# Kernel optimization log

Hardware: AMD Instinct MI355X
Metric: run time of the kernel (lower is better)

## Reference

```python
import jax, jax.numpy as jnp
import numpy as np

N, NFEAT, NHID, NCLASS, NIDX = 200000, 512, 128, 70, 10000


def normalize_l2(X):
    # row L2-normalize; norm is detached in the original (stop_gradient),
    # inf scale (zero rows) mapped to 0
    rownorm = jax.lax.stop_gradient(jnp.linalg.norm(X, axis=1, keepdims=True))
    scale = jnp.where(rownorm > 0, 1.0 / rownorm, 0.0)
    return X * scale


def setup_inputs() -> dict:
    key = jax.random.key(0)
    ks = jax.random.split(key, 9)
    x = jax.random.normal(ks[0], (N, NFEAT), dtype=jnp.float32)
    simple_features = jax.random.normal(ks[1], (N, NFEAT), dtype=jnp.float32)
    idx = jax.random.randint(ks[2], (NIDX,), 0, N)
    s = 0.05
    W0 = jax.random.normal(ks[3], (NHID, NFEAT), dtype=jnp.float32) * s
    W1 = jax.random.normal(ks[4], (NHID, NFEAT), dtype=jnp.float32) * s
    G1 = jax.random.normal(ks[5], (NHID, NHID), dtype=jnp.float32) * s
    G2 = jax.random.normal(ks[6], (NHID, NHID), dtype=jnp.float32) * s
    GT = jax.random.normal(ks[7], (NHID, 2 * NHID), dtype=jnp.float32) * s
    Wc = jax.random.normal(ks[8], (NCLASS, NHID), dtype=jnp.float32) * s
    return {"x": x, "simple_features": simple_features, "idx": idx,
            "W0": W0, "W1": W1, "G1": G1, "G2": G2, "GT": GT, "Wc": Wc}


def reference(x, simple_features, idx, W0, W1, G1, G2, GT, Wc):
    x = normalize_l2(x)                      # [N, nfeat]
    sf = normalize_l2(simple_features)       # [N, nfeat]
    # dropout/dropout_adj are identity (p=0)
    layer_inner = jax.nn.relu(x @ W0.T)      # [N, nhid]
    lay_simple = jax.nn.relu(sf @ W1.T)      # [N, nhid]
    gate1 = layer_inner @ G1.T               # [N, nhid]
    gate2 = lay_simple @ G2.T                # [N, nhid]
    gate = jax.nn.sigmoid(jnp.concatenate([gate1, gate2], axis=1) @ GT.T)
    fix_inner = (1.0 - gate) * layer_inner + gate * lay_simple
    fix_inner = normalize_l2(fix_inner)
    logits = jax.nn.relu(fix_inner @ Wc.T)   # [N, nclass]
    return jax.nn.log_softmax(logits, axis=-1)[idx]
```

## Files before the change

### kernel.cpp

```cpp
#include <hip/hip_runtime.h>
#include <math.h>

#define NFEAT  512
#define NHID   128
#define NCLASS 70
#define NIDX   10000
#define NTILE  625
#define HELEMS (2u * NIDX * NHID)
#define GELEMS (2u * NIDX * NHID)
#define WIMG_ELEMS (2u * 128 * 512)
#define SMALL_ELEMS 74496u
#define WS_NEED ((size_t)(HELEMS + GELEMS + WIMG_ELEMS + SMALL_ELEMS) * 2)

typedef float  f32x4  __attribute__((ext_vector_type(4)));
typedef __bf16 bf16x8 __attribute__((ext_vector_type(8)));

static __device__ __forceinline__ unsigned short f2bf(float f) {
    unsigned u = __builtin_bit_cast(unsigned, f);
    u += 0x7fffu + ((u >> 16) & 1u);
    return (unsigned short)(u >> 16);
}
static __device__ __forceinline__ float bf2f(unsigned short h) {
    unsigned u = ((unsigned)h) << 16;
    return __builtin_bit_cast(float, u);
}
static __device__ __forceinline__ bf16x8 pack8(float4 a, float4 b) {
    bf16x8 r;
    r[0] = (__bf16)a.x; r[1] = (__bf16)a.y; r[2] = (__bf16)a.z; r[3] = (__bf16)a.w;
    r[4] = (__bf16)b.x; r[5] = (__bf16)b.y; r[6] = (__bf16)b.z; r[7] = (__bf16)b.w;
    return r;
}
static __device__ __forceinline__ bf16x8 pack8s(float4 a, float4 b, float s) {
    bf16x8 r;
    r[0] = (__bf16)(a.x * s); r[1] = (__bf16)(a.y * s); r[2] = (__bf16)(a.z * s); r[3] = (__bf16)(a.w * s);
    r[4] = (__bf16)(b.x * s); r[5] = (__bf16)(b.y * s); r[6] = (__bf16)(b.z * s); r[7] = (__bf16)(b.w * s);
    return r;
}
static __device__ __forceinline__ f32x4 MFMA(bf16x8 a, bf16x8 b, f32x4 c) {
    return __builtin_amdgcn_mfma_f32_16x16x32_bf16(a, b, c, 0, 0, 0);
}
static __device__ __forceinline__ bf16x8 ldsAx(const unsigned short* base, int row, int colb, int rstride) {
    return *(const bf16x8*)((const char*)base + row * rstride + (colb ^ ((row & 7) << 4)));
}
static __device__ __forceinline__ void ldsW1(unsigned short* base, int row, int col, unsigned short v) {
    *(unsigned short*)((char*)base + row * 256 + ((col * 2) ^ ((row & 7) << 4))) = v;
}
static __device__ __forceinline__ float ldsR1(const unsigned short* base, int row, int col) {
    return bf2f(*(const unsigned short*)((const char*)base + row * 256 + ((col * 2) ^ ((row & 7) << 4))));
}

__global__ void prep_weights(const float* __restrict__ W0, const float* __restrict__ W1,
                             const float* __restrict__ G1, const float* __restrict__ G2,
                             const float* __restrict__ GT, const float* __restrict__ Wc,
                             unsigned short* __restrict__ wsWimg,
                             unsigned short* __restrict__ wsSmall) {
    int i = blockIdx.x * 256 + threadIdx.x;
    if (i < 16384) {
        int t = i >> 13;
        int r = i & 8191;
        int n = r >> 6, k8 = r & 63;
        const float* src = (t ? W1 : W0) + (size_t)n * NFEAT + k8 * 8;
        float4 a = ((const float4*)src)[0], b = ((const float4*)src)[1];
        char* dst = (char*)wsWimg + t * 131072 + n * 1024 + ((k8 * 16) ^ ((n & 7) << 4));
        *(bf16x8*)dst = pack8(a, b);
    } else {
        int i4 = i - 16384;
        if (i4 >= 18624) return;
        const float* src; int base4, dstb;
        if      (i4 < 4096)  { src = G1; base4 = 0;     dstb = 0; }
        else if (i4 < 8192)  { src = G2; base4 = 4096;  dstb = 16384; }
        else if (i4 < 16384) { src = GT; base4 = 8192;  dstb = 32768; }
        else                 { src = Wc; base4 = 16384; dstb = 65536; }
        float4 v = ((const float4*)src)[i4 - base4];
        ushort4 o;
        o.x = f2bf(v.x); o.y = f2bf(v.y); o.z = f2bf(v.z); o.w = f2bf(v.w);
        *(ushort4*)(wsSmall + dstb + (size_t)(i4 - base4) * 4) = o;
    }
}

__global__ __launch_bounds__(512) void stageBC(
    const float* __restrict__ x, const float* __restrict__ sf,
    const int* __restrict__ idx,
    const unsigned short* __restrict__ wsWimg,
    const unsigned short* __restrict__ wsSmall,
    unsigned short* __restrict__ wsH,
    unsigned short* __restrict__ wsG)
{
    __shared__ __align__(16) unsigned short Wl[65536];
    __shared__ __align__(16) unsigned short Xl[8192];
    __shared__ __align__(16) unsigned short Hl[2048];
    __shared__ __align__(16) unsigned short Gl[2048];

    const int tid  = threadIdx.x;
    const int w    = tid >> 6;
    const int lane = tid & 63;
    const int ln   = lane & 15, lg = lane >> 4;
    const int bid  = blockIdx.x;
    const int t    = bid / 125, tb = bid % 125;
    const int tile0 = tb * 5;
    const float* XS = t ? sf : x;
    const f32x4 zero4 = {0.f, 0.f, 0.f, 0.f};

    float4 ga0, ga1, gb0, gb1;
    {
        int r0 = idx[tile0 * 16 + w];
        int r1 = idx[tile0 * 16 + w + 8];
        const float4* p0 = (const float4*)(XS + (size_t)r0 * NFEAT + lane * 8);
        const float4* p1 = (const float4*)(XS + (size_t)r1 * NFEAT + lane * 8);
        ga0 = p0[0]; ga1 = p0[1];
        gb0 = p1[0]; gb1 = p1[1];
    }
    bf16x8 cf[4];
    {
        const unsigned short* Gsm = wsSmall + t * 16384;
        #pragma unroll
        for (int kc = 0; kc < 4; ++kc)
            cf[kc] = *(const bf16x8*)(Gsm + (size_t)(w * 16 + ln) * NHID + kc * 32 + lg * 8);
    }
    {
        const uint4* src = (const uint4*)((const char*)wsWimg + (size_t)t * 131072);
        uint4* dst = (uint4*)Wl;
        #pragma unroll
        for (int i = 0; i < 16; ++i) dst[tid + i * 512] = src[tid + i * 512];
    }
    auto putX = [&](int m, float4 a, float4 b) {
        float ss = a.x*a.x + a.y*a.y + a.z*a.z + a.w*a.w
                 + b.x*b.x + b.y*b.y + b.z*b.z + b.w*b.w;
        #pragma unroll
        for (int d = 1; d < 64; d <<= 1) ss += __shfl_xor(ss, d);
        float scl = (ss > 0.f) ? (1.f / sqrtf(ss)) : 0.f;
        *(bf16x8*)((char*)Xl + m * 1024 + ((lane * 16) ^ ((m & 7) << 4))) = pack8s(a, b, scl);
    };
    putX(w,     ga0, ga1);
    putX(w + 8, gb0, gb1);
    __syncthreads();

    for (int it = 0; it < 5; ++it) {
        float4 na0, na1, nb0, nb1;
        if (it < 4) {
            int tile = tile0 + it + 1;
            int r0 = idx[tile * 16 + w];
            int r1 = idx[tile * 16 + w + 8];
            const float4* p0 = (const float4*)(XS + (size_t)r0 * NFEAT + lane * 8);
            const float4* p1 = (const float4*)(XS + (size_t)r1 * NFEAT + lane * 8);
            na0 = p0[0]; na1 = p0[1];
            nb0 = p1[0]; nb1 = p1[1];
        }
        f32x4 accE = zero4, accO = zero4;
        #pragma unroll
        for (int kc = 0; kc < 16; ++kc) {
            bf16x8 a = ldsAx(Xl, ln,          kc * 64 + lg * 16, 1024);
            bf16x8 b = ldsAx(Wl, w * 16 + ln, kc * 64 + lg * 16, 1024);
            if (kc & 1) accO = MFMA(a, b, accO); else accE = MFMA(a, b, accE);
        }
        f32x4 acc = accE + accO;
        #pragma unroll
        for (int rg = 0; rg < 4; ++rg)
            ldsW1(Hl, lg * 4 + rg, w * 16 + ln, f2bf(fmaxf(acc[rg], 0.f)));
        __syncthreads();

        f32x4 aC = zero4;
        #pragma unroll
        for (int kc = 0; kc < 4; ++kc) {
            bf16x8 a = ldsAx(Hl, ln, kc * 64 + lg * 16, 256);
            aC = MFMA(a, cf[kc], aC);
        }
        if (tid < 256) {
            int tile = tile0 + it;
            ((uint4*)(wsH + ((size_t)t * NIDX + (size_t)tile * 16) * NHID))[tid]
                = ((const uint4*)Hl)[tid];
        }
        if (it < 4) {
            putX(w,     na0, na1);
            putX(w + 8, nb0, nb1);
        }
        #pragma unroll
        for (int rg = 0; rg < 4; ++rg)
            ldsW1(Gl, lg * 4 + rg, w * 16 + ln, f2bf(aC[rg]));
        __syncthreads();

        if (tid < 256) {
            int tile = tile0 + it;
            ((uint4*)(wsG + ((size_t)t * NIDX + (size_t)tile * 16) * NHID))[tid]
                = ((const uint4*)Gl)[tid];
        }
    }
}

__global__ __launch_bounds__(512) void tailDE5(
    const unsigned short* __restrict__ wsSmall,
    const unsigned short* __restrict__ wsH,
    const unsigned short* __restrict__ wsG,
    float* __restrict__ out)
{
    __shared__ __align__(16) char SM[102400];
    __shared__ float scl2s[5][16];

    unsigned short* Hb = (unsigned short*)SM;
    unsigned short* Gb = (unsigned short*)(SM + 40960);
    unsigned short* FX = (unsigned short*)(SM + 81920);
    float* LOGb = (float*)SM;

    const unsigned short* GTp = wsSmall + 32768;
    const unsigned short* Wcp = wsSmall + 65536;

    const int tid  = threadIdx.x;
    const int w    = tid >> 6;
    const int lane = tid & 63;
    const int ln   = lane & 15, lg = lane >> 4;
    const int tile0 = blockIdx.x * 5;
    const f32x4 zero4 = {0.f, 0.f, 0.f, 0.f};

    #pragma unroll
    for (int i = 0; i < 5; ++i) {
        int q = tid + i * 512;
        int seg = q >> 8, r = q & 255;
        int ti = seg >> 1, tt = seg & 1;
        size_t off = ((size_t)tt * NIDX + (size_t)(tile0 + ti) * 16) * NHID;
        ((uint4*)Hb)[q] = ((const uint4*)(wsH + off))[r];
        ((uint4*)Gb)[q] = ((const uint4*)(wsG + off))[r];
    }
    const int nD = w * 16 + ln;
    bf16x8 gt[8];
    #pragma unroll
    for (int kc = 0; kc < 8; ++kc)
        gt[kc] = *(const bf16x8*)(GTp + (size_t)nD * (2 * NHID) + kc * 32 + lg * 8);
    const int ccE = nD;
    const int ccl = (ccE < NCLASS) ? ccE : 0;
    bf16x8 wcf[4];
    #pragma unroll
    for (int kc = 0; kc < 4; ++kc)
        wcf[kc] = *(const bf16x8*)(Wcp + (size_t)ccl * NHID + kc * 32 + lg * 8);
    __syncthreads();

    #pragma unroll
    for (int ti = 0; ti < 5; ++ti) {
        f32x4 aE = zero4, aO = zero4;
        #pragma unroll
        for (int kc = 0; kc < 8; ++kc) {
            const unsigned short* As = Gb + ti * 4096 + (kc >> 2) * 2048;
            bf16x8 a = ldsAx(As, ln, (kc & 3) * 64 + lg * 16, 256);
            if (kc & 1) aO = MFMA(a, gt[kc], aO); else aE = MFMA(a, gt[kc], aE);
        }
        f32x4 accD = aE + aO;
        #pragma unroll
        for (int rg = 0; rg < 4; ++rg) {
            int m = lg * 4 + rg;
            float g  = 1.f / (1.f + __expf(-accD[rg]));
            float h0 = ldsR1(Hb + ti * 4096,        m, nD);
            float h1 = ldsR1(Hb + ti * 4096 + 2048, m, nD);
            ldsW1(FX + ti * 2048, m, nD, f2bf((1.f - g) * h0 + g * h1));
        }
    }
    __syncthreads();

    {
        int rr = tid >> 4, sl = tid & 15;
        #pragma unroll
        for (int j = 0; j < 3; ++j) {
            int rs = j * 32 + rr;
            if (rs < 80) {
                int ti = rs >> 4, r = rs & 15;
                bf16x8 v = ldsAx(FX + ti * 2048, r, sl * 16, 256);
                float ss = 0.f;
                #pragma unroll
                for (int jj = 0; jj < 8; ++jj) { float f = (float)v[jj]; ss += f * f; }
                ss += __shfl_xor(ss, 1); ss += __shfl_xor(ss, 2);
                ss += __shfl_xor(ss, 4); ss += __shfl_xor(ss, 8);
                if (sl == 0) scl2s[ti][r] = (ss > 0.f) ? (1.f / sqrtf(ss)) : 0.f;
            }
        }
    }
    __syncthreads();

    if (w < 5) {
        const bool live = (ccE < NCLASS);
        bf16x8 bfz;
        #pragma unroll
        for (int j = 0; j < 8; ++j) bfz[j] = (__bf16)0.f;
        #pragma unroll
        for (int ti = 0; ti < 5; ++ti) {
            f32x4 accE = zero4;
            #pragma unroll
            for (int kc = 0; kc < 4; ++kc) {
                bf16x8 a = ldsAx(FX + ti * 2048, ln, kc * 64 + lg * 16, 256);
                accE = MFMA(a, live ? wcf[kc] : bfz, accE);
            }
            if (live) {
                float* LO = LOGb + ti * 1280;
                #pragma unroll
                for (int rg = 0; rg < 4; ++rg) {
                    int m = lg * 4 + rg;
                    LO[m * 80 + ccE] = fmaxf(accE[rg] * scl2s[ti][m], 0.f);
                }
            }
        }
    }
    __syncthreads();

    {
        int rr = tid >> 4, l16 = tid & 15;
        #pragma unroll
        for (int j = 0; j < 3; ++j) {
            int rs = j * 32 + rr;
            if (rs < 80) {
                int ti = rs >> 4, r = rs & 15;
                const float* LO = LOGb + ti * 1280 + r * 80;
                float v[5];
                #pragma unroll
                for (int jj = 0; jj < 5; ++jj) {
                    int c = l16 + jj * 16;
                    v[jj] = (c < NCLASS) ? LO[c] : -1e30f;
                }
                float mx = v[0];
                #pragma unroll
                for (int jj = 1; jj < 5; ++jj) mx = fmaxf(mx, v[jj]);
                mx = fmaxf(mx, __shfl_xor(mx, 1)); mx = fmaxf(mx, __shfl_xor(mx, 2));
                mx = fmaxf(mx, __shfl_xor(mx, 4)); mx = fmaxf(mx, __shfl_xor(mx, 8));
                float se = 0.f;
                #pragma unroll
                for (int jj = 0; jj < 5; ++jj) {
                    int c = l16 + jj * 16;
                    if (c < NCLASS) se += __expf(v[jj] - mx);
                }
                se += __shfl_xor(se, 1); se += __shfl_xor(se, 2);
                se += __shfl_xor(se, 4); se += __shfl_xor(se, 8);
                float lz = mx + __logf(se);
                size_t orow = (size_t)(tile0 + ti) * 16 + r;
                #pragma unroll
                for (int jj = 0; jj < 5; ++jj) {
                    int c = l16 + jj * 16;
                    if (c < NCLASS) out[orow * NCLASS + c] = v[jj] - lz;
                }
            }
        }
    }
}

static __device__ __forceinline__ bf16x8 bfragF(const float* p, size_t off) {
    const float4* q = (const float4*)(p + off);
    return pack8(q[0], q[1]);
}
__global__ __launch_bounds__(512) void hyper_fb(
    const float* __restrict__ x, const float* __restrict__ sf,
    const int* __restrict__ idx,
    const float* __restrict__ W0, const float* __restrict__ W1,
    const float* __restrict__ G1, const float* __restrict__ G2,
    const float* __restrict__ GT, const float* __restrict__ Wc,
    float* __restrict__ out)
{
    __shared__ __align__(16) unsigned short Xbuf[2][16][NFEAT];
    __shared__ __align__(16) unsigned short Hbuf[2][16][NHID];
    __shared__ float scl2[16];
    unsigned short* G12 = &Xbuf[0][0][0];
    unsigned short* FIX = &Xbuf[0][0][0] + 4096;
    float*          LOG = (float*)(&Xbuf[0][0][0] + 6144);

    const int tid = threadIdx.x, bid = blockIdx.x;
    const int w = tid >> 6, lane = tid & 63;
    const int ln = lane & 15, lg = lane >> 4;
    const int tB = w >> 2, nq = w & 3;
    const f32x4 zero4 = {0.f, 0.f, 0.f, 0.f};

    {
        char* xb = (char*)&Xbuf[0][0][0];
        #pragma unroll
        for (int j = 0; j < 4; ++j) {
            int p = w * 4 + j, t = p >> 4, m = p & 15;
            int ri = idx[bid * 16 + m];
            const float4* q = (const float4*)((t ? sf : x) + (size_t)ri * NFEAT + lane * 8);
            float4 a = q[0], b = q[1];
            float ss = a.x*a.x + a.y*a.y + a.z*a.z + a.w*a.w
                     + b.x*b.x + b.y*b.y + b.z*b.z + b.w*b.w;
            #pragma unroll
            for (int d = 1; d < 64; d <<= 1) ss += __shfl_xor(ss, d);
            float scl = (ss > 0.f) ? (1.f / sqrtf(ss)) : 0.f;
            int soff = t * 16384 + m * 1024 + ((lane * 16) ^ ((m & 7) << 4));
            *(bf16x8*)(xb + soff) = pack8s(a, b, scl);
        }
    }
    __syncthreads();
    {
        const float* Wp = tB ? W1 : W0;
        f32x4 acc0 = zero4, acc1 = zero4;
        const unsigned short* Xb = (const unsigned short*)((const char*)&Xbuf[0][0][0] + tB * 16384);
        #pragma unroll
        for (int kc = 0; kc < 16; ++kc) {
            bf16x8 a = ldsAx(Xb, ln, kc * 64 + lg * 16, 1024);
            acc0 = MFMA(a, bfragF(Wp, (size_t)(nq * 32 + ln) * NFEAT + kc * 32 + lg * 8), acc0);
            acc1 = MFMA(a, bfragF(Wp, (size_t)(nq * 32 + 16 + ln) * NFEAT + kc * 32 + lg * 8), acc1);
        }
        unsigned short* Hb = &Hbuf[tB][0][0];
        #pragma unroll
        for (int rg = 0; rg < 4; ++rg) {
            int m = lg * 4 + rg;
            ldsW1(Hb, m, nq * 32 + ln,      f2bf(fmaxf(acc0[rg], 0.f)));
            ldsW1(Hb, m, nq * 32 + 16 + ln, f2bf(fmaxf(acc1[rg], 0.f)));
        }
    }
    __syncthreads();
    {
        const float* Gp = tB ? G2 : G1;
        const unsigned short* Hs = &Hbuf[tB][0][0];
        f32x4 accC[2] = {zero4, zero4};
        #pragma unroll
        for (int kc = 0; kc < 4; ++kc) {
            bf16x8 a = ldsAx(Hs, ln, kc * 64 + lg * 16, 256);
            accC[0] = MFMA(a, bfragF(Gp, (size_t)(nq * 32 + ln) * NHID + kc * 32 + lg * 8), accC[0]);
            accC[1] = MFMA(a, bfragF(Gp, (size_t)(nq * 32 + 16 + ln) * NHID + kc * 32 + lg * 8), accC[1]);
        }
        unsigned short* Gd = G12 + tB * 2048;
        #pragma unroll
        for (int nt = 0; nt < 2; ++nt)
            #pragma unroll
            for (int rg = 0; rg < 4; ++rg) {
                int m = lg * 4 + rg;
                ldsW1(Gd, m, nq * 32 + nt * 16 + ln, f2bf(accC[nt][rg]));
            }
    }
    __syncthreads();
    {
        f32x4 accD = zero4;
        const int n = w * 16 + ln;
        #pragma unroll
        for (int kc = 0; kc < 8; ++kc) {
            const unsigned short* As = G12 + (kc >> 2) * 2048;
            bf16x8 a = ldsAx(As, ln, (kc & 3) * 64 + lg * 16, 256);
            accD = MFMA(a, bfragF(GT, (size_t)n * (2 * NHID) + kc * 32 + lg * 8), accD);
        }
        #pragma unroll
        for (int rg = 0; rg < 4; ++rg) {
            int m = lg * 4 + rg;
            float g  = 1.f / (1.f + __expf(-accD[rg]));
            float h0 = ldsR1(&Hbuf[0][0][0], m, n);
            float h1 = ldsR1(&Hbuf[1][0][0], m, n);
            ldsW1(FIX, m, n, f2bf((1.f - g) * h0 + g * h1));
        }
    }
    __syncthreads();
    if (tid < 256) {
        int r = tid >> 4, sl = tid & 15;
        bf16x8 v = ldsAx(FIX, r, sl * 16, 256);
        float ss = 0.f;
        #pragma unroll
        for (int j = 0; j < 8; ++j) { float f = (float)v[j]; ss += f * f; }
        ss += __shfl_xor(ss, 1); ss += __shfl_xor(ss, 2);
        ss += __shfl_xor(ss, 4); ss += __shfl_xor(ss, 8);
        if (sl == 0) scl2[r] = (ss > 0.f) ? (1.f / sqrtf(ss)) : 0.f;
    }
    __syncthreads();
    if (w < 5) {
        const int cc = w * 16 + ln;
        bf16x8 bfz;
        #pragma unroll
        for (int j = 0; j < 8; ++j) bfz[j] = (__bf16)0.f;
        f32x4 accE = zero4;
        #pragma unroll
        for (int kc = 0; kc < 4; ++kc) {
            bf16x8 a = ldsAx(FIX, ln, kc * 64 + lg * 16, 256);
            bf16x8 b = (cc < NCLASS) ? bfragF(Wc, (size_t)cc * NHID + kc * 32 + lg * 8) : bfz;
            accE = MFMA(a, b, accE);
        }
        #pragma unroll
        for (int rg = 0; rg < 4; ++rg) {
            int m = lg * 4 + rg;
            float v = fmaxf(accE[rg] * scl2[m], 0.f);
            LOG[m * 80 + cc] = (cc < NCLASS) ? v : -1e30f;
        }
    }
    __syncthreads();
    {
        const int r = tid >> 5, l32 = tid & 31;
        float v0 = LOG[r * 80 + l32];
        float v1 = LOG[r * 80 + 32 + l32];
        float v2 = (l32 < 16) ? LOG[r * 80 + 64 + l32] : -1e30f;
        float mx = fmaxf(fmaxf(v0, v1), v2);
        #pragma unroll
        for (int d = 1; d < 32; d <<= 1) mx = fmaxf(mx, __shfl_xor(mx, d, 32));
        float se = __expf(v0 - mx) + __expf(v1 - mx) + ((l32 < 16) ? __expf(v2 - mx) : 0.f);
        #pragma unroll
        for (int d = 1; d < 32; d <<= 1) se += __shfl_xor(se, d, 32);
        float lz = mx + __logf(se);
        size_t orow = (size_t)bid * 16 + r;
        out[orow * NCLASS + l32] = v0 - lz;
        if (l32 + 32 < NCLASS) out[orow * NCLASS + 32 + l32] = v1 - lz;
        if (l32 + 64 < NCLASS) out[orow * NCLASS + 64 + l32] = v2 - lz;
    }
}

extern "C" void kernel_launch(void* const* d_in, const int* in_sizes, int n_in,
                              void* d_out, int out_size, void* d_ws, size_t ws_size,
                              hipStream_t stream)
{
    const float* x   = (const float*)d_in[0];
    const float* sf  = (const float*)d_in[1];
    const int*   idx = (const int*)d_in[2];
    const float* W0  = (const float*)d_in[3];
    const float* W1  = (const float*)d_in[4];
    const float* G1  = (const float*)d_in[5];
    const float* G2  = (const float*)d_in[6];
    const float* GT  = (const float*)d_in[7];
    const float* Wc  = (const float*)d_in[8];
    float* out = (float*)d_out;

    if (ws_size >= WS_NEED) {
        unsigned short* wsH     = (unsigned short*)d_ws;
        unsigned short* wsG     = wsH + HELEMS;
        unsigned short* wsWimg  = wsG + GELEMS;
        unsigned short* wsSmall = wsWimg + WIMG_ELEMS;
        prep_weights<<<dim3(137), dim3(256), 0, stream>>>(W0, W1, G1, G2, GT, Wc, wsWimg, wsSmall);
        stageBC<<<dim3(250), dim3(512), 0, stream>>>(x, sf, idx, wsWimg, wsSmall, wsH, wsG);
        tailDE5<<<dim3(125), dim3(512), 0, stream>>>(wsSmall, wsH, wsG, out);
    } else {
        hyper_fb<<<dim3(NTILE), dim3(512), 0, stream>>>(
            x, sf, idx, W0, W1, G1, G2, GT, Wc, out);
    }
}
```

Measured before the change: 37.02 us.

## Keep first-layer weights in registers as MFMA fragments, one tile per block

The first-layer weights are pre-packed into a per-wave, per-lane MFMA fragment layout so each wave loads its 16 B-fragments straight from global memory into registers. This replaces the 128 KB shared-memory weight staging. With the large LDS buffer gone, the kernel launches one block per 16-row tile per branch (1250 blocks instead of 250 blocks looping over 5 tiles), aiming for more occupancy and parallelism. The cost is that every block re-reads its 16 KB per-wave weight slice from L2, and the cross-iteration prefetch of the next tile's rows is lost.

```diff
diff --git a/kernel.cpp b/kernel.cpp
--- a/kernel.cpp
+++ b/kernel.cpp
@@ -8,9 +8,9 @@
 #define NTILE  625
 #define HELEMS (2u * NIDX * NHID)
 #define GELEMS (2u * NIDX * NHID)
-#define WIMG_ELEMS (2u * 128 * 512)
+#define WFRAG_ELEMS (2u * 128 * 512)
 #define SMALL_ELEMS 74496u
-#define WS_NEED ((size_t)(HELEMS + GELEMS + WIMG_ELEMS + SMALL_ELEMS) * 2)
+#define WS_NEED ((size_t)(HELEMS + GELEMS + WFRAG_ELEMS + SMALL_ELEMS) * 2)
 
 typedef float  f32x4  __attribute__((ext_vector_type(4)));
 typedef __bf16 bf16x8 __attribute__((ext_vector_type(8)));
@@ -52,17 +52,18 @@
 __global__ void prep_weights(const float* __restrict__ W0, const float* __restrict__ W1,
                              const float* __restrict__ G1, const float* __restrict__ G2,
                              const float* __restrict__ GT, const float* __restrict__ Wc,
-                             unsigned short* __restrict__ wsWimg,
+                             unsigned short* __restrict__ wsWfrag,
                              unsigned short* __restrict__ wsSmall) {
     int i = blockIdx.x * 256 + threadIdx.x;
     if (i < 16384) {
         int t = i >> 13;
         int r = i & 8191;
-        int n = r >> 6, k8 = r & 63;
-        const float* src = (t ? W1 : W0) + (size_t)n * NFEAT + k8 * 8;
+        int w = r >> 10, kc = (r >> 6) & 15, lane = r & 63;
+        int n   = w * 16 + (lane & 15);
+        int col = kc * 32 + (lane >> 4) * 8;
+        const float* src = (t ? W1 : W0) + (size_t)n * NFEAT + col;
         float4 a = ((const float4*)src)[0], b = ((const float4*)src)[1];
-        char* dst = (char*)wsWimg + t * 131072 + n * 1024 + ((k8 * 16) ^ ((n & 7) << 4));
-        *(bf16x8*)dst = pack8(a, b);
+        *(bf16x8*)(wsWfrag + (size_t)i * 8) = pack8(a, b);
     } else {
         int i4 = i - 16384;
         if (i4 >= 18624) return;
@@ -78,15 +79,14 @@
     }
 }
 
-__global__ __launch_bounds__(512) void stageBC(
+__global__ __launch_bounds__(512) void stageBC_reg(
     const float* __restrict__ x, const float* __restrict__ sf,
     const int* __restrict__ idx,
-    const unsigned short* __restrict__ wsWimg,
+    const unsigned short* __restrict__ wsWfrag,
     const unsigned short* __restrict__ wsSmall,
     unsigned short* __restrict__ wsH,
     unsigned short* __restrict__ wsG)
 {
-    __shared__ __align__(16) unsigned short Wl[65536];
     __shared__ __align__(16) unsigned short Xl[8192];
     __shared__ __align__(16) unsigned short Hl[2048];
     __shared__ __align__(16) unsigned short Gl[2048];
@@ -96,32 +96,32 @@
     const int lane = tid & 63;
     const int ln   = lane & 15, lg = lane >> 4;
     const int bid  = blockIdx.x;
-    const int t    = bid / 125, tb = bid % 125;
-    const int tile0 = tb * 5;
+    const int t    = bid & 1, tile = bid >> 1;
     const float* XS = t ? sf : x;
     const f32x4 zero4 = {0.f, 0.f, 0.f, 0.f};
 
     float4 ga0, ga1, gb0, gb1;
     {
-        int r0 = idx[tile0 * 16 + w];
-        int r1 = idx[tile0 * 16 + w + 8];
+        int r0 = idx[tile * 16 + w];
+        int r1 = idx[tile * 16 + w + 8];
         const float4* p0 = (const float4*)(XS + (size_t)r0 * NFEAT + lane * 8);
         const float4* p1 = (const float4*)(XS + (size_t)r1 * NFEAT + lane * 8);
         ga0 = p0[0]; ga1 = p0[1];
         gb0 = p1[0]; gb1 = p1[1];
     }
+    bf16x8 wf[16];
+    {
+        const unsigned short* wb = wsWfrag + ((size_t)(t * 8 + w) * 16) * 512 + lane * 8;
+        #pragma unroll
+        for (int kc = 0; kc < 16; ++kc)
+            wf[kc] = *(const bf16x8*)(wb + kc * 512);
+    }
     bf16x8 cf[4];
     {
         const unsigned short* Gsm = wsSmall + t * 16384;
         #pragma unroll
         for (int kc = 0; kc < 4; ++kc)
             cf[kc] = *(const bf16x8*)(Gsm + (size_t)(w * 16 + ln) * NHID + kc * 32 + lg * 8);
-    }
-    {
-        const uint4* src = (const uint4*)((const char*)wsWimg + (size_t)t * 131072);
-        uint4* dst = (uint4*)Wl;
-        #pragma unroll
-        for (int i = 0; i < 16; ++i) dst[tid + i * 512] = src[tid + i * 512];
     }
     auto putX = [&](int m, float4 a, float4 b) {
         float ss = a.x*a.x + a.y*a.y + a.z*a.z + a.w*a.w
@@ -135,30 +135,21 @@
     putX(w + 8, gb0, gb1);
     __syncthreads();
 
-    for (int it = 0; it < 5; ++it) {
-        float4 na0, na1, nb0, nb1;
-        if (it < 4) {
-            int tile = tile0 + it + 1;
-            int r0 = idx[tile * 16 + w];
-            int r1 = idx[tile * 16 + w + 8];
-            const float4* p0 = (const float4*)(XS + (size_t)r0 * NFEAT + lane * 8);
-            const float4* p1 = (const float4*)(XS + (size_t)r1 * NFEAT + lane * 8);
-            na0 = p0[0]; na1 = p0[1];
-            nb0 = p1[0]; nb1 = p1[1];
-        }
+    {
         f32x4 accE = zero4, accO = zero4;
         #pragma unroll
         for (int kc = 0; kc < 16; ++kc) {
-            bf16x8 a = ldsAx(Xl, ln,          kc * 64 + lg * 16, 1024);
-            bf16x8 b = ldsAx(Wl, w * 16 + ln, kc * 64 + lg * 16, 1024);
-            if (kc & 1) accO = MFMA(a, b, accO); else accE = MFMA(a, b, accE);
+            bf16x8 a = ldsAx(Xl, ln, kc * 64 + lg * 16, 1024);
+            if (kc & 1) accO = MFMA(a, wf[kc], accO); else accE = MFMA(a, wf[kc], accE);
         }
         f32x4 acc = accE + accO;
         #pragma unroll
         for (int rg = 0; rg < 4; ++rg)
             ldsW1(Hl, lg * 4 + rg, w * 16 + ln, f2bf(fmaxf(acc[rg], 0.f)));
-        __syncthreads();
-
+    }
+    __syncthreads();
+
+    {
         f32x4 aC = zero4;
         #pragma unroll
         for (int kc = 0; kc < 4; ++kc) {
@@ -166,24 +157,18 @@
             aC = MFMA(a, cf[kc], aC);
         }
         if (tid < 256) {
-            int tile = tile0 + it;
             ((uint4*)(wsH + ((size_t)t * NIDX + (size_t)tile * 16) * NHID))[tid]
                 = ((const uint4*)Hl)[tid];
         }
-        if (it < 4) {
-            putX(w,     na0, na1);
-            putX(w + 8, nb0, nb1);
-        }
         #pragma unroll
         for (int rg = 0; rg < 4; ++rg)
             ldsW1(Gl, lg * 4 + rg, w * 16 + ln, f2bf(aC[rg]));
-        __syncthreads();
-
-        if (tid < 256) {
-            int tile = tile0 + it;
-            ((uint4*)(wsG + ((size_t)t * NIDX + (size_t)tile * 16) * NHID))[tid]
-                = ((const uint4*)Gl)[tid];
-        }
+    }
+    __syncthreads();
+
+    if (tid < 256) {
+        ((uint4*)(wsG + ((size_t)t * NIDX + (size_t)tile * 16) * NHID))[tid]
+            = ((const uint4*)Gl)[tid];
     }
 }
 
@@ -506,10 +491,10 @@
     if (ws_size >= WS_NEED) {
         unsigned short* wsH     = (unsigned short*)d_ws;
         unsigned short* wsG     = wsH + HELEMS;
-        unsigned short* wsWimg  = wsG + GELEMS;
-        unsigned short* wsSmall = wsWimg + WIMG_ELEMS;
-        prep_weights<<<dim3(137), dim3(256), 0, stream>>>(W0, W1, G1, G2, GT, Wc, wsWimg, wsSmall);
-        stageBC<<<dim3(250), dim3(512), 0, stream>>>(x, sf, idx, wsWimg, wsSmall, wsH, wsG);
+        unsigned short* wsWfrag = wsG + GELEMS;
+        unsigned short* wsSmall = wsWfrag + WFRAG_ELEMS;
+        prep_weights<<<dim3(137), dim3(256), 0, stream>>>(W0, W1, G1, G2, GT, Wc, wsWfrag, wsSmall);
+        stageBC_reg<<<dim3(2 * NTILE), dim3(512), 0, stream>>>(x, sf, idx, wsWfrag, wsSmall, wsH, wsG);
         tailDE5<<<dim3(125), dim3(512), 0, stream>>>(wsSmall, wsH, wsG, out);
     } else {
         hyper_fb<<<dim3(NTILE), dim3(512), 0, stream>>>(
```

New measurement: 37.01 us (median of 2 runs). About the same (-0.0%).
